# Kernel tuning notes

Measured on AMD Instinct MI355X. Metric: run time of the kernel, lower is better.

## Reference

```python
import jax, jax.numpy as jnp
import numpy as np

M, K, N = 131072, 1024, 512


def setup_inputs() -> dict:
    key = jax.random.key(0)
    k1, k2, k3, k4, k5 = jax.random.split(key, 5)
    scale = 0.02
    return {
        "x": jax.random.normal(k1, (M, K), dtype=jnp.float32),
        "w0": jax.random.uniform(k2, (K,), dtype=jnp.float32, minval=0.9, maxval=1.1),
        "w1": jax.random.normal(k3, (K, N), dtype=jnp.float32) * scale,
        "w2": jax.random.normal(k4, (K, N), dtype=jnp.float32) * scale,
        "w3": jax.random.normal(k5, (N, K), dtype=jnp.float32) * scale,
    }


def reference(x, w0, w1, w2, w3):
    # RMSNorm (no eps, matching the kernel): l = rsqrt(mean(x^2))
    l = jax.lax.rsqrt(jnp.sum(x * x, axis=-1) / K)          # [M]
    x1 = x * l[:, None] * w0[None, :]                        # [M, K]
    x2 = x1 @ w1                                             # gate   [M, N]
    y2 = x1 @ w2                                             # up     [M, N]
    x3 = jax.nn.silu(x2) * y2                                # SiLU-gate [M, N]
    out = x3 @ w3                                            # down   [M, K] (skip_connection=False)
    return out
```

## Files before the change

kernel.cpp:

```cpp
#include <hip/hip_runtime.h>
#include <cstdint>

typedef __attribute__((ext_vector_type(4))) float f32x4;
typedef __attribute__((ext_vector_type(8))) short bf16x8;
typedef __attribute__((ext_vector_type(4))) short bf16x4;

#define DEV static __device__ __forceinline__

DEV unsigned short f2bf(float f) {
    union { float f; unsigned int u; } v; v.f = f;
    unsigned int u = v.u;
    return (unsigned short)((u + 0x7FFFu + ((u >> 16) & 1u)) >> 16);
}

DEV void async_cp16(const void* g, void* l) {
    __builtin_amdgcn_global_load_lds(
        (const __attribute__((address_space(1))) unsigned int*)g,
        (__attribute__((address_space(3))) unsigned int*)l,
        16, 0, 0);
}

DEV void stage_half(const unsigned short* __restrict__ g, long kofs,
                    unsigned short* l, int tid, int gpitch) {
#pragma unroll
    for (int i = 0; i < 2; ++i) {
        int c = i * 512 + tid;
        int row = c >> 3;
        int ss = (c & 7) ^ (row & 7);
        async_cp16(g + (long)row * gpitch + kofs + ss * 8,
                   l + (i * 512 + (tid & 448)) * 8);
    }
}

DEV bf16x8 ldsrd(const unsigned short* base, int r, int q) {
    return *(const bf16x8*)&base[r * 64 + ((q ^ (r & 7)) << 3)];
}

template <int NT>
DEV void gemm256(const unsigned short* __restrict__ gA,
                 const unsigned short* __restrict__ gB,
                 const int gpitch, unsigned short* lds,
                 f32x4 (&acc)[8][4], const int tid) {
    const int lane = tid & 63;
    const int wv = tid >> 6;
    const int wr = wv >> 2;
    const int wcq = wv & 3;
    const int lhi = lane >> 4, llo = lane & 15;
    const int hb = wcq >> 1;
    const int br0 = (wcq & 1) * 64;

    const unsigned short* lA0 = lds + (0 * 2 + wr) * 8192;
    const unsigned short* lA1 = lds + (1 * 2 + wr) * 8192;
    const unsigned short* lB0 = lds + 32768 + (0 * 2 + hb) * 8192;
    const unsigned short* lB1 = lds + 32768 + (1 * 2 + hb) * 8192;

#define MG(AF, BF, RI0, CJ0)                                                  \
    _Pragma("unroll") for (int kq = 0; kq < 2; ++kq)                          \
    _Pragma("unroll") for (int i = 0; i < 4; ++i)                             \
    _Pragma("unroll") for (int j = 0; j < 2; ++j)                             \
        acc[RI0 + i][CJ0 + j] = __builtin_amdgcn_mfma_f32_16x16x32_bf16(      \
            AF[kq][i], BF[kq][j], acc[RI0 + i][CJ0 + j], 0, 0, 0);

#define RD_AF0(L) _Pragma("unroll") for (int kq = 0; kq < 2; ++kq)            \
    _Pragma("unroll") for (int i = 0; i < 4; ++i)                             \
        af0[kq][i] = ldsrd(L, i * 16 + llo, kq * 4 + lhi);
#define RD_AF1(L) _Pragma("unroll") for (int kq = 0; kq < 2; ++kq)            \
    _Pragma("unroll") for (int i = 0; i < 4; ++i)                             \
        af1[kq][i] = ldsrd(L, 64 + i * 16 + llo, kq * 4 + lhi);
#define RD_BF0(L) _Pragma("unroll") for (int kq = 0; kq < 2; ++kq)            \
    _Pragma("unroll") for (int j = 0; j < 2; ++j)                             \
        bf0[kq][j] = ldsrd(L, br0 + j * 16 + llo, kq * 4 + lhi);
#define RD_BF1(L) _Pragma("unroll") for (int kq = 0; kq < 2; ++kq)            \
    _Pragma("unroll") for (int j = 0; j < 2; ++j)                             \
        bf1[kq][j] = ldsrd(L, br0 + 32 + j * 16 + llo, kq * 4 + lhi);

#define SA0(BUF, K) stage_half(gA, K, lds + ((BUF) * 2 + 0) * 8192, tid, gpitch);
#define SA1(BUF, K) stage_half(gA + (long)128 * gpitch, K, lds + ((BUF) * 2 + 1) * 8192, tid, gpitch);
#define SB0(BUF, K) stage_half(gB, K, lds + 32768 + ((BUF) * 2 + 0) * 8192, tid, gpitch);
#define SB1(BUF, K) stage_half(gB + (long)128 * gpitch, K, lds + 32768 + ((BUF) * 2 + 1) * 8192, tid, gpitch);

#define BAR __builtin_amdgcn_s_barrier();
#define SCB __builtin_amdgcn_sched_barrier(0);
#define LGKM0 asm volatile("s_waitcnt lgkmcnt(0)");
#define P1 __builtin_amdgcn_s_setprio(1);
#define P0 __builtin_amdgcn_s_setprio(0);
#define VM2 asm volatile("s_waitcnt vmcnt(2)" ::: "memory");
#define VM0 asm volatile("s_waitcnt vmcnt(0)" ::: "memory");

    SA0(0, 0) SA1(0, 0) SB0(0, 0) SB1(0, 0)
    SA0(1, 64)
    VM2
    BAR

    bf16x8 af0[2][4], af1[2][4], bf0[2][2], bf1[2][2];

    for (int it = 0; it < NT / 2; ++it) {
        const long kO  = (long)(2 * it + 1) * 64;
        const long kE2 = (long)(2 * it + 2) * 64;
        const long kO2 = (long)(2 * it + 3) * 64;
        const bool pf = (it + 1 < NT / 2);

        RD_AF0(lA0) RD_BF0(lB0)
        SA1(1, kO)
        BAR LGKM0 SCB
        P1 MG(af0, bf0, 0, 0) P0
        BAR
        RD_BF1(lB0)
        SB0(1, kO)
        BAR LGKM0 SCB
        P1 MG(af0, bf1, 0, 2) P0
        BAR
        RD_AF1(lA0)
        SB1(1, kO)
        BAR LGKM0 SCB
        P1 MG(af1, bf0, 4, 0) P0
        BAR
        if (pf) { SA0(0, kE2) }
        BAR
        P1 MG(af1, bf1, 4, 2) P0
        if (pf) { VM2 } else { VM0 }
        BAR SCB

        RD_AF0(lA1) RD_BF0(lB1)
        if (pf) { SA1(0, kE2) }
        BAR LGKM0 SCB
        P1 MG(af0, bf0, 0, 0) P0
        BAR
        RD_BF1(lB1)
        if (pf) { SB0(0, kE2) }
        BAR LGKM0 SCB
        P1 MG(af0, bf1, 0, 2) P0
        BAR
        RD_AF1(lA1)
        if (pf) { SB1(0, kE2) }
        BAR LGKM0 SCB
        P1 MG(af1, bf0, 4, 0) P0
        BAR
        if (pf) { SA0(1, kO2) }
        BAR
        P1 MG(af1, bf1, 4, 2) P0
        if (pf) { VM2 }
        BAR SCB
    }
#undef MG
#undef RD_AF0
#undef RD_AF1
#undef RD_BF0
#undef RD_BF1
#undef SA0
#undef SA1
#undef SB0
#undef SB1
#undef BAR
#undef SCB
#undef LGKM0
#undef P1
#undef P0
#undef VM2
#undef VM0
}

__global__ void prep_w(const float* __restrict__ w0, const float* __restrict__ w1,
                       const float* __restrict__ w2, const float* __restrict__ w3,
                       unsigned short* __restrict__ w12t, unsigned short* __restrict__ w3t) {
    int t = blockIdx.x * 256 + threadIdx.x;
    if (t < 1048576) {
        int n = t >> 10, k = t & 1023;
        const float* src = (n & 1) ? w2 : w1;
        w12t[t] = f2bf(w0[k] * src[k * 512 + (n >> 1)]);
    } else {
        int idx = t - 1048576;
        int j = idx >> 9, n = idx & 511;
        w3t[idx] = f2bf(w3[n * 1024 + j]);
    }
}

__global__ __launch_bounds__(256)
void prep_x(const float* __restrict__ x, unsigned short* __restrict__ xb) {
    const int wv = threadIdx.x >> 6, lane = threadIdx.x & 63;
    const int stride = gridDim.x * 4;
    for (int row = blockIdx.x * 4 + wv; row < 131072; row += stride) {
        const float* xr = x + (long)row * 1024;
        f32x4 v[4];
        float s = 0.f;
#pragma unroll
        for (int c = 0; c < 4; ++c) {
            v[c] = *(const f32x4*)(xr + c * 256 + lane * 4);
            s += v[c].x * v[c].x + v[c].y * v[c].y + v[c].z * v[c].z + v[c].w * v[c].w;
        }
#pragma unroll
        for (int off = 32; off > 0; off >>= 1) s += __shfl_xor(s, off, 64);
        float l = rsqrtf(s * (1.0f / 1024.0f));
        unsigned short* xo = xb + (long)row * 1024;
#pragma unroll
        for (int c = 0; c < 4; ++c) {
            bf16x4 b;
            b.x = (short)f2bf(v[c].x * l);
            b.y = (short)f2bf(v[c].y * l);
            b.z = (short)f2bf(v[c].z * l);
            b.w = (short)f2bf(v[c].w * l);
            *(bf16x4*)(xo + c * 256 + lane * 4) = b;
        }
    }
}

__global__ __launch_bounds__(512, 2)
void gate_gemm(const unsigned short* __restrict__ xb,
               const unsigned short* __restrict__ w12t,
               unsigned short* __restrict__ x3) {
    __shared__ unsigned short lds[65536];
    const int tid = threadIdx.x;
    const int lane = tid & 63;
    const int wv = tid >> 6;
    const int wr = wv >> 2, wcq = wv & 3;
    const int lhi = lane >> 4, llo = lane & 15;

    int bid = blockIdx.x;
    int wgid = (bid & 7) * 256 + (bid >> 3);
    const int mt = wgid >> 2, nt = wgid & 3;

    f32x4 acc[8][4];
#pragma unroll
    for (int i = 0; i < 8; ++i)
#pragma unroll
        for (int j = 0; j < 4; ++j) acc[i][j] = (f32x4){0.f, 0.f, 0.f, 0.f};

    gemm256<16>(xb + (long)mt * 256 * 1024, w12t + (long)nt * 256 * 1024,
                1024, lds, acc, tid);

#pragma unroll
    for (int ri = 0; ri < 8; ++ri)
#pragma unroll
        for (int rr = 0; rr < 4; ++rr) {
            int R = wr * 128 + ri * 16 + lhi * 4 + rr;
#pragma unroll
            for (int cj = 0; cj < 4; ++cj) {
                float v = acc[ri][cj][rr];
                float p = __shfl_xor(v, 1, 64);
                float g = (lane & 1) ? p : v;
                float u = (lane & 1) ? v : p;
                float s = (g / (1.0f + __expf(-g))) * u;
                if (!(lane & 1))
                    lds[R * 136 + wcq * 32 + cj * 8 + (llo >> 1)] = f2bf(s);
            }
        }
    __syncthreads();
    unsigned short* xg = x3 + (long)(mt * 256) * 512 + nt * 128;
#pragma unroll
    for (int i = 0; i < 8; ++i) {
        int c = i * 512 + tid;
        int row = c >> 4, ch = c & 15;
        *(bf16x8*)(xg + (long)row * 512 + ch * 8) = *(const bf16x8*)&lds[row * 136 + ch * 8];
    }
}

__global__ __launch_bounds__(512, 2)
void down_gemm(const unsigned short* __restrict__ x3,
               const unsigned short* __restrict__ w3t,
               float* __restrict__ out) {
    __shared__ unsigned short lds[65536];
    const int tid = threadIdx.x;
    const int lane = tid & 63;
    const int wv = tid >> 6;
    const int wr = wv >> 2, wcq = wv & 3;
    const int lhi = lane >> 4, llo = lane & 15;

    int bid = blockIdx.x;
    int wgid = (bid & 7) * 256 + (bid >> 3);
    const int mt = wgid >> 2, nt = wgid & 3;

    f32x4 acc[8][4];
#pragma unroll
    for (int i = 0; i < 8; ++i)
#pragma unroll
        for (int j = 0; j < 4; ++j) acc[i][j] = (f32x4){0.f, 0.f, 0.f, 0.f};

    gemm256<8>(x3 + (long)mt * 256 * 512, w3t + (long)nt * 256 * 512,
               512, lds, acc, tid);

    float* op = out + (long)(mt * 256) * 1024 + nt * 256;
#pragma unroll
    for (int ri = 0; ri < 8; ++ri)
#pragma unroll
        for (int rr = 0; rr < 4; ++rr) {
            int R = wr * 128 + ri * 16 + lhi * 4 + rr;
#pragma unroll
            for (int cj = 0; cj < 4; ++cj)
                op[(long)R * 1024 + wcq * 64 + cj * 16 + llo] = acc[ri][cj][rr];
        }
}

extern "C" void kernel_launch(void* const* d_in, const int* in_sizes, int n_in,
                              void* d_out, int out_size, void* d_ws, size_t ws_size,
                              hipStream_t stream) {
    const float* x  = (const float*)d_in[0];
    const float* w0 = (const float*)d_in[1];
    const float* w1 = (const float*)d_in[2];
    const float* w2 = (const float*)d_in[3];
    const float* w3 = (const float*)d_in[4];
    float* out = (float*)d_out;

    unsigned short* w12t = (unsigned short*)d_ws;
    unsigned short* w3t  = w12t + 1024 * 1024;
    unsigned short* x3   = w3t + 1024 * 512;
    unsigned short* xb   = x3 + (size_t)131072 * 512;

    prep_w<<<dim3(6144), dim3(256), 0, stream>>>(w0, w1, w2, w3, w12t, w3t);
    prep_x<<<dim3(2048), dim3(256), 0, stream>>>(x, xb);
    gate_gemm<<<dim3(2048), dim3(512), 0, stream>>>(xb, w12t, x3);
    down_gemm<<<dim3(2048), dim3(512), 0, stream>>>(x3, w3t, out);
}
```

Measured before the change: 697.7 us.

## Fuse RMSNorm prep into gate GEMM by loading fp32 x and converting in-kernel

Removes the separate prep_x kernel. The gate GEMM now loads fp32 x rows directly into registers, converts them to bf16, and writes them into swizzled LDS while accumulating the sum of squares. The per-row rsqrt scale is applied to the accumulators after the GEMM, before the SiLU gate. This eliminates the bf16 xb round trip through HBM (one write plus one read), but each of the four N-tile blocks now reads fp32 x, doubling A-side read bytes, and the pipeline waits on vmcnt(0) each tile, which reduces overlap.

```diff
diff --git a/kernel.cpp b/kernel.cpp
--- a/kernel.cpp
+++ b/kernel.cpp
@@ -1,9 +1,11 @@
 #include <hip/hip_runtime.h>
+#include <hip/hip_bf16.h>
 #include <cstdint>
 
 typedef __attribute__((ext_vector_type(4))) float f32x4;
 typedef __attribute__((ext_vector_type(8))) short bf16x8;
 typedef __attribute__((ext_vector_type(4))) short bf16x4;
+typedef __attribute__((ext_vector_type(4))) unsigned int u32x4;
 
 #define DEV static __device__ __forceinline__
 
@@ -11,6 +13,10 @@
     union { float f; unsigned int u; } v; v.f = f;
     unsigned int u = v.u;
     return (unsigned short)((u + 0x7FFFu + ((u >> 16) & 1u)) >> 16);
+}
+
+DEV unsigned int pkbf(float a, float b) {
+    return ((unsigned int)f2bf(b) << 16) | f2bf(a);
 }
 
 DEV void async_cp16(const void* g, void* l) {
@@ -35,6 +41,35 @@
 DEV bf16x8 ldsrd(const unsigned short* base, int r, int q) {
     return *(const bf16x8*)&base[r * 64 + ((q ^ (r & 7)) << 3)];
 }
+
+#define BAR __builtin_amdgcn_s_barrier();
+#define SCB __builtin_amdgcn_sched_barrier(0);
+#define LGKM0 asm volatile("s_waitcnt lgkmcnt(0)");
+#define P1 __builtin_amdgcn_s_setprio(1);
+#define P0 __builtin_amdgcn_s_setprio(0);
+#define VM0 asm volatile("s_waitcnt vmcnt(0)" ::: "memory");
+#define VM2 asm volatile("s_waitcnt vmcnt(2)" ::: "memory");
+#define VM8 asm volatile("s_waitcnt vmcnt(8)" ::: "memory");
+
+#define MG(AF, BF, RI0, CJ0)                                                  \
+    _Pragma("unroll") for (int kq = 0; kq < 2; ++kq)                          \
+    _Pragma("unroll") for (int i = 0; i < 4; ++i)                             \
+    _Pragma("unroll") for (int j = 0; j < 2; ++j)                             \
+        acc[RI0 + i][CJ0 + j] = __builtin_amdgcn_mfma_f32_16x16x32_bf16(      \
+            AF[kq][i], BF[kq][j], acc[RI0 + i][CJ0 + j], 0, 0, 0);
+
+#define RD_AF0(L) _Pragma("unroll") for (int kq = 0; kq < 2; ++kq)            \
+    _Pragma("unroll") for (int i = 0; i < 4; ++i)                             \
+        af0[kq][i] = ldsrd(L, i * 16 + llo, kq * 4 + lhi);
+#define RD_AF1(L) _Pragma("unroll") for (int kq = 0; kq < 2; ++kq)            \
+    _Pragma("unroll") for (int i = 0; i < 4; ++i)                             \
+        af1[kq][i] = ldsrd(L, 64 + i * 16 + llo, kq * 4 + lhi);
+#define RD_BF0(L) _Pragma("unroll") for (int kq = 0; kq < 2; ++kq)            \
+    _Pragma("unroll") for (int j = 0; j < 2; ++j)                             \
+        bf0[kq][j] = ldsrd(L, br0 + j * 16 + llo, kq * 4 + lhi);
+#define RD_BF1(L) _Pragma("unroll") for (int kq = 0; kq < 2; ++kq)            \
+    _Pragma("unroll") for (int j = 0; j < 2; ++j)                             \
+        bf1[kq][j] = ldsrd(L, br0 + 32 + j * 16 + llo, kq * 4 + lhi);
 
 template <int NT>
 DEV void gemm256(const unsigned short* __restrict__ gA,
@@ -54,38 +89,10 @@
     const unsigned short* lB0 = lds + 32768 + (0 * 2 + hb) * 8192;
     const unsigned short* lB1 = lds + 32768 + (1 * 2 + hb) * 8192;
 
-#define MG(AF, BF, RI0, CJ0)                                                  \
-    _Pragma("unroll") for (int kq = 0; kq < 2; ++kq)                          \
-    _Pragma("unroll") for (int i = 0; i < 4; ++i)                             \
-    _Pragma("unroll") for (int j = 0; j < 2; ++j)                             \
-        acc[RI0 + i][CJ0 + j] = __builtin_amdgcn_mfma_f32_16x16x32_bf16(      \
-            AF[kq][i], BF[kq][j], acc[RI0 + i][CJ0 + j], 0, 0, 0);
-
-#define RD_AF0(L) _Pragma("unroll") for (int kq = 0; kq < 2; ++kq)            \
-    _Pragma("unroll") for (int i = 0; i < 4; ++i)                             \
-        af0[kq][i] = ldsrd(L, i * 16 + llo, kq * 4 + lhi);
-#define RD_AF1(L) _Pragma("unroll") for (int kq = 0; kq < 2; ++kq)            \
-    _Pragma("unroll") for (int i = 0; i < 4; ++i)                             \
-        af1[kq][i] = ldsrd(L, 64 + i * 16 + llo, kq * 4 + lhi);
-#define RD_BF0(L) _Pragma("unroll") for (int kq = 0; kq < 2; ++kq)            \
-    _Pragma("unroll") for (int j = 0; j < 2; ++j)                             \
-        bf0[kq][j] = ldsrd(L, br0 + j * 16 + llo, kq * 4 + lhi);
-#define RD_BF1(L) _Pragma("unroll") for (int kq = 0; kq < 2; ++kq)            \
-    _Pragma("unroll") for (int j = 0; j < 2; ++j)                             \
-        bf1[kq][j] = ldsrd(L, br0 + 32 + j * 16 + llo, kq * 4 + lhi);
-
 #define SA0(BUF, K) stage_half(gA, K, lds + ((BUF) * 2 + 0) * 8192, tid, gpitch);
 #define SA1(BUF, K) stage_half(gA + (long)128 * gpitch, K, lds + ((BUF) * 2 + 1) * 8192, tid, gpitch);
 #define SB0(BUF, K) stage_half(gB, K, lds + 32768 + ((BUF) * 2 + 0) * 8192, tid, gpitch);
 #define SB1(BUF, K) stage_half(gB + (long)128 * gpitch, K, lds + 32768 + ((BUF) * 2 + 1) * 8192, tid, gpitch);
-
-#define BAR __builtin_amdgcn_s_barrier();
-#define SCB __builtin_amdgcn_sched_barrier(0);
-#define LGKM0 asm volatile("s_waitcnt lgkmcnt(0)");
-#define P1 __builtin_amdgcn_s_setprio(1);
-#define P0 __builtin_amdgcn_s_setprio(0);
-#define VM2 asm volatile("s_waitcnt vmcnt(2)" ::: "memory");
-#define VM0 asm volatile("s_waitcnt vmcnt(0)" ::: "memory");
 
     SA0(0, 0) SA1(0, 0) SB0(0, 0) SB1(0, 0)
     SA0(1, 64)
@@ -142,22 +149,10 @@
         if (pf) { VM2 }
         BAR SCB
     }
-#undef MG
-#undef RD_AF0
-#undef RD_AF1
-#undef RD_BF0
-#undef RD_BF1
 #undef SA0
 #undef SA1
 #undef SB0
 #undef SB1
-#undef BAR
-#undef SCB
-#undef LGKM0
-#undef P1
-#undef P0
-#undef VM2
-#undef VM0
 }
 
 __global__ void prep_w(const float* __restrict__ w0, const float* __restrict__ w1,
@@ -175,67 +170,133 @@
     }
 }
 
-__global__ __launch_bounds__(256)
-void prep_x(const float* __restrict__ x, unsigned short* __restrict__ xb) {
-    const int wv = threadIdx.x >> 6, lane = threadIdx.x & 63;
-    const int stride = gridDim.x * 4;
-    for (int row = blockIdx.x * 4 + wv; row < 131072; row += stride) {
-        const float* xr = x + (long)row * 1024;
-        f32x4 v[4];
-        float s = 0.f;
-#pragma unroll
-        for (int c = 0; c < 4; ++c) {
-            v[c] = *(const f32x4*)(xr + c * 256 + lane * 4);
-            s += v[c].x * v[c].x + v[c].y * v[c].y + v[c].z * v[c].z + v[c].w * v[c].w;
-        }
-#pragma unroll
-        for (int off = 32; off > 0; off >>= 1) s += __shfl_xor(s, off, 64);
-        float l = rsqrtf(s * (1.0f / 1024.0f));
-        unsigned short* xo = xb + (long)row * 1024;
-#pragma unroll
-        for (int c = 0; c < 4; ++c) {
-            bf16x4 b;
-            b.x = (short)f2bf(v[c].x * l);
-            b.y = (short)f2bf(v[c].y * l);
-            b.z = (short)f2bf(v[c].z * l);
-            b.w = (short)f2bf(v[c].w * l);
-            *(bf16x4*)(xo + c * 256 + lane * 4) = b;
-        }
-    }
-}
-
 __global__ __launch_bounds__(512, 2)
-void gate_gemm(const unsigned short* __restrict__ xb,
+void gate_gemm(const float* __restrict__ x,
                const unsigned short* __restrict__ w12t,
                unsigned short* __restrict__ x3) {
     __shared__ unsigned short lds[65536];
+    __shared__ float spart[1024];
+    __shared__ float lrow[256];
+
     const int tid = threadIdx.x;
     const int lane = tid & 63;
     const int wv = tid >> 6;
     const int wr = wv >> 2, wcq = wv & 3;
     const int lhi = lane >> 4, llo = lane & 15;
+    const int hb = wcq >> 1;
+    const int br0 = (wcq & 1) * 64;
 
     int bid = blockIdx.x;
     int wgid = (bid & 7) * 256 + (bid >> 3);
     const int mt = wgid >> 2, nt = wgid & 3;
 
+    const unsigned short* gB = w12t + (long)nt * 256 * 1024;
+    const int arow = tid >> 2;
+    const int acol = tid & 3;
+    const float* gxr0 = x + (long)(mt * 256 + arow) * 1024 + acol * 16;
+    const float* gxr1 = gxr0 + (long)128 * 1024;
+    const int ws0 = (((acol * 2)     ^ (arow & 7)) << 3);
+    const int ws1 = (((acol * 2 + 1) ^ (arow & 7)) << 3);
+
+    f32x4 ar[2][4];
+    float sq0 = 0.f, sq1 = 0.f;
+
+#define ALOAD(KOFS) { _Pragma("unroll") for (int c = 0; c < 4; ++c) {          \
+        ar[0][c] = *(const f32x4*)(gxr0 + (KOFS) + c * 4);                     \
+        ar[1][c] = *(const f32x4*)(gxr1 + (KOFS) + c * 4); } }
+
+#define ACVT(D) { _Pragma("unroll") for (int h2 = 0; h2 < 2; ++h2) {           \
+        float s = 0.f; unsigned int pk[8];                                     \
+        _Pragma("unroll") for (int c = 0; c < 4; ++c) {                        \
+            f32x4 v = ar[h2][c];                                               \
+            s += v.x * v.x + v.y * v.y + v.z * v.z + v.w * v.w;                \
+            pk[c * 2]     = pkbf(v.x, v.y);                                    \
+            pk[c * 2 + 1] = pkbf(v.z, v.w); }                                  \
+        if (h2 == 0) sq0 += s; else sq1 += s;                                  \
+        unsigned short* dst = lds + ((D) * 2 + h2) * 8192 + arow * 64;         \
+        *(u32x4*)(dst + ws0) = (u32x4){pk[0], pk[1], pk[2], pk[3]};            \
+        *(u32x4*)(dst + ws1) = (u32x4){pk[4], pk[5], pk[6], pk[7]}; } }
+
+#define SB0G(BUF, K) stage_half(gB, K, lds + 32768 + ((BUF) * 2 + 0) * 8192, tid, 1024);
+#define SB1G(BUF, K) stage_half(gB + (long)128 * 1024, K, lds + 32768 + ((BUF) * 2 + 1) * 8192, tid, 1024);
+
     f32x4 acc[8][4];
 #pragma unroll
     for (int i = 0; i < 8; ++i)
 #pragma unroll
         for (int j = 0; j < 4; ++j) acc[i][j] = (f32x4){0.f, 0.f, 0.f, 0.f};
 
-    gemm256<16>(xb + (long)mt * 256 * 1024, w12t + (long)nt * 256 * 1024,
-                1024, lds, acc, tid);
+    ALOAD(0)
+    SB0G(0, 0) SB1G(0, 0)
+    ACVT(0)
+    ALOAD(64)
+    LGKM0
+    VM8
+    BAR SCB
+
+    bf16x8 af0[2][4], af1[2][4], bf0[2][2], bf1[2][2];
+
+#define GTILE(CUR, NXT, T)                                                     \
+    {                                                                          \
+        const unsigned short* lA = lds + ((CUR) * 2 + wr) * 8192;              \
+        const unsigned short* lB = lds + 32768 + ((CUR) * 2 + hb) * 8192;      \
+        const bool pf = (T) + 1 < 16;                                          \
+        const bool al = ((T) >= 1) && pf;                                      \
+        const long k1 = (long)((T) + 1) * 64;                                  \
+                                                                      \
+        RD_AF0(lA) RD_BF0(lB)                                                  \
+        BAR LGKM0 SCB                                                          \
+        P1 MG(af0, bf0, 0, 0) P0                                               \
+        BAR                                                                    \
+                                                                      \
+        RD_BF1(lB)                                                             \
+        if (pf) { SB0G(NXT, k1) SB1G(NXT, k1) }                                \
+        BAR LGKM0 SCB                                                          \
+        P1 MG(af0, bf1, 0, 2) P0                                               \
+        BAR                                                                    \
+                                                                      \
+        RD_AF1(lA)                                                             \
+        if (al) { ALOAD(k1 * 1) }                                              \
+        BAR LGKM0 SCB                                                          \
+        P1 MG(af1, bf0, 4, 0) P0                                               \
+        BAR                                                                    \
+                                                                      \
+        P1 MG(af1, bf1, 4, 2) P0                                               \
+        if (pf) { ACVT(NXT) }                                                  \
+        LGKM0                                                                  \
+        if (pf) { VM0 }                                                        \
+        BAR SCB                                                                \
+    }
+
+#pragma unroll
+    for (int it = 0; it < 8; ++it) {
+        GTILE(0, 1, 2 * it)
+        GTILE(1, 0, 2 * it + 1)
+    }
+#undef GTILE
+#undef ALOAD
+#undef ACVT
+#undef SB0G
+#undef SB1G
+
+    spart[arow * 4 + acol] = sq0;
+    spart[(128 + arow) * 4 + acol] = sq1;
+    __syncthreads();
+    if (tid < 256) {
+        float s = spart[tid * 4] + spart[tid * 4 + 1] + spart[tid * 4 + 2] + spart[tid * 4 + 3];
+        lrow[tid] = rsqrtf(s * (1.0f / 1024.0f));
+    }
+    __syncthreads();
 
 #pragma unroll
     for (int ri = 0; ri < 8; ++ri)
 #pragma unroll
         for (int rr = 0; rr < 4; ++rr) {
             int R = wr * 128 + ri * 16 + lhi * 4 + rr;
+            float l = lrow[R];
 #pragma unroll
             for (int cj = 0; cj < 4; ++cj) {
-                float v = acc[ri][cj][rr];
+                float v = acc[ri][cj][rr] * l;
                 float p = __shfl_xor(v, 1, 64);
                 float g = (lane & 1) ? p : v;
                 float u = (lane & 1) ? v : p;
@@ -303,10 +364,8 @@
     unsigned short* w12t = (unsigned short*)d_ws;
     unsigned short* w3t  = w12t + 1024 * 1024;
     unsigned short* x3   = w3t + 1024 * 512;
-    unsigned short* xb   = x3 + (size_t)131072 * 512;
 
     prep_w<<<dim3(6144), dim3(256), 0, stream>>>(w0, w1, w2, w3, w12t, w3t);
-    prep_x<<<dim3(2048), dim3(256), 0, stream>>>(x, xb);
-    gate_gemm<<<dim3(2048), dim3(512), 0, stream>>>(xb, w12t, x3);
+    gate_gemm<<<dim3(2048), dim3(512), 0, stream>>>(x, w12t, x3);
     down_gemm<<<dim3(2048), dim3(512), 0, stream>>>(x3, w3t, out);
 }
```

Measured after the change: 906.1 us. 1.3x slower.

## Switch GEMM core to 32x32x16 bf16 MFMA with new LDS swizzle

Applied to the files above, without the earlier changes.

Replaces the 16x16x32 MFMA tiling with 32x32x16 bf16 MFMA instructions in the shared 256x256 GEMM core. Each wave now holds 4x2 32x32 accumulators. The LDS swizzle gains an extra XOR term so the new 32-lane read pattern avoids bank conflicts. Both epilogues are remapped to the new accumulator layout. The intent is fewer MFMA issues and LDS reads per FLOP, at the cost of changed register pressure and more complex index mapping.

```diff
diff --git a/kernel.cpp b/kernel.cpp
--- a/kernel.cpp
+++ b/kernel.cpp
@@ -2,6 +2,7 @@
 #include <cstdint>
 
 typedef __attribute__((ext_vector_type(4))) float f32x4;
+typedef __attribute__((ext_vector_type(16))) float f32x16;
 typedef __attribute__((ext_vector_type(8))) short bf16x8;
 typedef __attribute__((ext_vector_type(4))) short bf16x4;
 
@@ -20,79 +21,81 @@
         16, 0, 0);
 }
 
-DEV void stage_half(const unsigned short* __restrict__ g, long kofs,
-                    unsigned short* l, int tid, int gpitch) {
-#pragma unroll
-    for (int i = 0; i < 2; ++i) {
-        int c = i * 512 + tid;
-        int row = c >> 3;
-        int ss = (c & 7) ^ (row & 7);
-        async_cp16(g + (long)row * gpitch + kofs + ss * 8,
-                   l + (i * 512 + (tid & 448)) * 8);
-    }
-}
-
-DEV bf16x8 ldsrd(const unsigned short* base, int r, int q) {
-    return *(const bf16x8*)&base[r * 64 + ((q ^ (r & 7)) << 3)];
-}
-
-template <int NT>
-DEV void gemm256(const unsigned short* __restrict__ gA,
-                 const unsigned short* __restrict__ gB,
-                 const int gpitch, unsigned short* lds,
-                 f32x4 (&acc)[8][4], const int tid) {
-    const int lane = tid & 63;
-    const int wv = tid >> 6;
-    const int wr = wv >> 2;
-    const int wcq = wv & 3;
-    const int lhi = lane >> 4, llo = lane & 15;
-    const int hb = wcq >> 1;
-    const int br0 = (wcq & 1) * 64;
-
-    const unsigned short* lA0 = lds + (0 * 2 + wr) * 8192;
-    const unsigned short* lA1 = lds + (1 * 2 + wr) * 8192;
-    const unsigned short* lB0 = lds + 32768 + (0 * 2 + hb) * 8192;
-    const unsigned short* lB1 = lds + 32768 + (1 * 2 + hb) * 8192;
-
-#define MG(AF, BF, RI0, CJ0)                                                  \
-    _Pragma("unroll") for (int kq = 0; kq < 2; ++kq)                          \
-    _Pragma("unroll") for (int i = 0; i < 4; ++i)                             \
-    _Pragma("unroll") for (int j = 0; j < 2; ++j)                             \
-        acc[RI0 + i][CJ0 + j] = __builtin_amdgcn_mfma_f32_16x16x32_bf16(      \
-            AF[kq][i], BF[kq][j], acc[RI0 + i][CJ0 + j], 0, 0, 0);
-
-#define RD_AF0(L) _Pragma("unroll") for (int kq = 0; kq < 2; ++kq)            \
-    _Pragma("unroll") for (int i = 0; i < 4; ++i)                             \
-        af0[kq][i] = ldsrd(L, i * 16 + llo, kq * 4 + lhi);
-#define RD_AF1(L) _Pragma("unroll") for (int kq = 0; kq < 2; ++kq)            \
-    _Pragma("unroll") for (int i = 0; i < 4; ++i)                             \
-        af1[kq][i] = ldsrd(L, 64 + i * 16 + llo, kq * 4 + lhi);
-#define RD_BF0(L) _Pragma("unroll") for (int kq = 0; kq < 2; ++kq)            \
-    _Pragma("unroll") for (int j = 0; j < 2; ++j)                             \
-        bf0[kq][j] = ldsrd(L, br0 + j * 16 + llo, kq * 4 + lhi);
-#define RD_BF1(L) _Pragma("unroll") for (int kq = 0; kq < 2; ++kq)            \
-    _Pragma("unroll") for (int j = 0; j < 2; ++j)                             \
-        bf1[kq][j] = ldsrd(L, br0 + 32 + j * 16 + llo, kq * 4 + lhi);
-
-#define SA0(BUF, K) stage_half(gA, K, lds + ((BUF) * 2 + 0) * 8192, tid, gpitch);
-#define SA1(BUF, K) stage_half(gA + (long)128 * gpitch, K, lds + ((BUF) * 2 + 1) * 8192, tid, gpitch);
-#define SB0(BUF, K) stage_half(gB, K, lds + 32768 + ((BUF) * 2 + 0) * 8192, tid, gpitch);
-#define SB1(BUF, K) stage_half(gB + (long)128 * gpitch, K, lds + 32768 + ((BUF) * 2 + 1) * 8192, tid, gpitch);
-
 #define BAR __builtin_amdgcn_s_barrier();
 #define SCB __builtin_amdgcn_sched_barrier(0);
 #define LGKM0 asm volatile("s_waitcnt lgkmcnt(0)");
 #define P1 __builtin_amdgcn_s_setprio(1);
 #define P0 __builtin_amdgcn_s_setprio(0);
+#define VM0 asm volatile("s_waitcnt vmcnt(0)" ::: "memory");
 #define VM2 asm volatile("s_waitcnt vmcnt(2)" ::: "memory");
-#define VM0 asm volatile("s_waitcnt vmcnt(0)" ::: "memory");
+
+DEV void stage_half(const unsigned short* __restrict__ g, long kofs,
+                    unsigned short* l, int tid, int gpitch) {
+#pragma unroll
+    for (int i = 0; i < 2; ++i) {
+        int c = i * 512 + tid;
+        int row = c >> 3;
+        int ss = (c & 7) ^ (row & 7) ^ ((row >> 3) & 3);
+        async_cp16(g + (long)row * gpitch + kofs + ss * 8,
+                   l + (i * 512 + (tid & 448)) * 8);
+    }
+}
+
+template <int NT>
+DEV void gemm256(const unsigned short* __restrict__ gA,
+                 const unsigned short* __restrict__ gB,
+                 const int gpitch, unsigned short* lds,
+                 f32x16 (&acc)[4][2], const int tid) {
+    const int lane = tid & 63;
+    const int wv = tid >> 6;
+    const int wr = wv >> 2, wcq = wv & 3;
+    const int lw = lane & 31, hi5 = lane >> 5;
+    const int hb = wcq >> 1;
+    const int brq = wcq & 1;
+    const int F = (lw & 7) ^ ((lw >> 3) & 3);
+
+    const char* lb = (const char*)lds;
+    int oA[4], oB[4];
+#pragma unroll
+    for (int ks = 0; ks < 4; ++ks) {
+        int q = (((ks * 2 + hi5) ^ F) << 4);
+        oA[ks] = wr * 16384 + lw * 128 + q;
+        oB[ks] = 65536 + hb * 16384 + brq * 8192 + lw * 128 + q;
+    }
+
+#define LD8(OFF) (*(const bf16x8*)(lb + (OFF)))
+#define RD_AF(MB, CO) _Pragma("unroll") for (int ks = 0; ks < 4; ++ks) {      \
+        af[0][ks] = LD8(oA[ks] + (CO) + (MB) * 4096);                         \
+        af[1][ks] = LD8(oA[ks] + (CO) + (MB) * 4096 + 4096); }
+#define RD_BFA(CO) _Pragma("unroll") for (int ks = 0; ks < 2; ++ks) {         \
+        bfA[0][ks] = LD8(oB[ks] + (CO));                                      \
+        bfA[1][ks] = LD8(oB[ks] + (CO) + 4096); }
+#define RD_BFB(CO) _Pragma("unroll") for (int ks = 0; ks < 2; ++ks) {         \
+        bfB[0][ks] = LD8(oB[ks + 2] + (CO));                                  \
+        bfB[1][ks] = LD8(oB[ks + 2] + (CO) + 4096); }
+
+#define MM(B_, KB0, MOFF)                                                     \
+    _Pragma("unroll") for (int ks = 0; ks < 2; ++ks)                          \
+    _Pragma("unroll") for (int m = 0; m < 2; ++m)                             \
+    _Pragma("unroll") for (int n = 0; n < 2; ++n)                             \
+        acc[(MOFF) + m][n] = __builtin_amdgcn_mfma_f32_32x32x16_bf16(         \
+            af[m][(KB0) + ks], B_[n][ks], acc[(MOFF) + m][n], 0, 0, 0);
+
+#define SA0(BUF, K) stage_half(gA, K, lds + ((BUF) * 2 + 0) * 8192, tid, gpitch);
+#define SA1(BUF, K) stage_half(gA + (long)128 * gpitch, K, lds + ((BUF) * 2 + 1) * 8192, tid, gpitch);
+#define SB0(BUF, K) stage_half(gB, K, lds + 32768 + ((BUF) * 2 + 0) * 8192, tid, gpitch);
+#define SB1(BUF, K) stage_half(gB + (long)128 * gpitch, K, lds + 32768 + ((BUF) * 2 + 1) * 8192, tid, gpitch);
 
     SA0(0, 0) SA1(0, 0) SB0(0, 0) SB1(0, 0)
-    SA0(1, 64)
-    VM2
-    BAR
-
-    bf16x8 af0[2][4], af1[2][4], bf0[2][2], bf1[2][2];
+    if (NT > 1) {
+        SA0(1, 64)
+        VM2
+    } else {
+        VM0
+    }
+    BAR SCB
+
+    bf16x8 af[2][4], bfA[2][2], bfB[2][2];
 
     for (int it = 0; it < NT / 2; ++it) {
         const long kO  = (long)(2 * it + 1) * 64;
@@ -100,64 +103,57 @@
         const long kO2 = (long)(2 * it + 3) * 64;
         const bool pf = (it + 1 < NT / 2);
 
-        RD_AF0(lA0) RD_BF0(lB0)
+        RD_AF(0, 0) RD_BFA(0)
         SA1(1, kO)
         BAR LGKM0 SCB
-        P1 MG(af0, bf0, 0, 0) P0
-        BAR
-        RD_BF1(lB0)
+        P1 MM(bfA, 0, 0) P0
+        BAR
+        RD_BFB(0)
         SB0(1, kO)
         BAR LGKM0 SCB
-        P1 MG(af0, bf1, 0, 2) P0
-        BAR
-        RD_AF1(lA0)
+        P1 MM(bfB, 2, 0) P0
+        BAR
+        RD_AF(2, 0)
         SB1(1, kO)
         BAR LGKM0 SCB
-        P1 MG(af1, bf0, 4, 0) P0
+        P1 MM(bfA, 0, 2) P0
         BAR
         if (pf) { SA0(0, kE2) }
         BAR
-        P1 MG(af1, bf1, 4, 2) P0
+        P1 MM(bfB, 2, 2) P0
         if (pf) { VM2 } else { VM0 }
         BAR SCB
 
-        RD_AF0(lA1) RD_BF0(lB1)
+        RD_AF(0, 32768) RD_BFA(32768)
         if (pf) { SA1(0, kE2) }
         BAR LGKM0 SCB
-        P1 MG(af0, bf0, 0, 0) P0
-        BAR
-        RD_BF1(lB1)
+        P1 MM(bfA, 0, 0) P0
+        BAR
+        RD_BFB(32768)
         if (pf) { SB0(0, kE2) }
         BAR LGKM0 SCB
-        P1 MG(af0, bf1, 0, 2) P0
-        BAR
-        RD_AF1(lA1)
+        P1 MM(bfB, 2, 0) P0
+        BAR
+        RD_AF(2, 32768)
         if (pf) { SB1(0, kE2) }
         BAR LGKM0 SCB
-        P1 MG(af1, bf0, 4, 0) P0
+        P1 MM(bfA, 0, 2) P0
         BAR
         if (pf) { SA0(1, kO2) }
         BAR
-        P1 MG(af1, bf1, 4, 2) P0
+        P1 MM(bfB, 2, 2) P0
         if (pf) { VM2 }
         BAR SCB
     }
-#undef MG
-#undef RD_AF0
-#undef RD_AF1
-#undef RD_BF0
-#undef RD_BF1
+#undef MM
+#undef LD8
+#undef RD_AF
+#undef RD_BFA
+#undef RD_BFB
 #undef SA0
 #undef SA1
 #undef SB0
 #undef SB1
-#undef BAR
-#undef SCB
-#undef LGKM0
-#undef P1
-#undef P0
-#undef VM2
-#undef VM0
 }
 
 __global__ void prep_w(const float* __restrict__ w0, const float* __restrict__ w1,
@@ -213,37 +209,38 @@
     const int lane = tid & 63;
     const int wv = tid >> 6;
     const int wr = wv >> 2, wcq = wv & 3;
-    const int lhi = lane >> 4, llo = lane & 15;
+    const int lw = lane & 31, hi5 = lane >> 5;
 
     int bid = blockIdx.x;
     int wgid = (bid & 7) * 256 + (bid >> 3);
     const int mt = wgid >> 2, nt = wgid & 3;
 
-    f32x4 acc[8][4];
-#pragma unroll
-    for (int i = 0; i < 8; ++i)
-#pragma unroll
-        for (int j = 0; j < 4; ++j) acc[i][j] = (f32x4){0.f, 0.f, 0.f, 0.f};
+    f32x16 acc[4][2];
+#pragma unroll
+    for (int i = 0; i < 4; ++i)
+#pragma unroll
+        for (int j = 0; j < 2; ++j)
+#pragma unroll
+            for (int r = 0; r < 16; ++r) acc[i][j][r] = 0.f;
 
     gemm256<16>(xb + (long)mt * 256 * 1024, w12t + (long)nt * 256 * 1024,
                 1024, lds, acc, tid);
 
 #pragma unroll
-    for (int ri = 0; ri < 8; ++ri)
-#pragma unroll
-        for (int rr = 0; rr < 4; ++rr) {
-            int R = wr * 128 + ri * 16 + lhi * 4 + rr;
-#pragma unroll
-            for (int cj = 0; cj < 4; ++cj) {
-                float v = acc[ri][cj][rr];
+    for (int m = 0; m < 4; ++m)
+#pragma unroll
+        for (int n = 0; n < 2; ++n)
+#pragma unroll
+            for (int reg = 0; reg < 16; ++reg) {
+                int R = wr * 128 + m * 32 + (reg & 3) + (reg >> 2) * 8 + hi5 * 4;
+                float v = acc[m][n][reg];
                 float p = __shfl_xor(v, 1, 64);
                 float g = (lane & 1) ? p : v;
                 float u = (lane & 1) ? v : p;
                 float s = (g / (1.0f + __expf(-g))) * u;
                 if (!(lane & 1))
-                    lds[R * 136 + wcq * 32 + cj * 8 + (llo >> 1)] = f2bf(s);
+                    lds[R * 136 + wcq * 32 + n * 16 + (lw >> 1)] = f2bf(s);
             }
-        }
     __syncthreads();
     unsigned short* xg = x3 + (long)(mt * 256) * 512 + nt * 128;
 #pragma unroll
@@ -263,31 +260,33 @@
     const int lane = tid & 63;
     const int wv = tid >> 6;
     const int wr = wv >> 2, wcq = wv & 3;
-    const int lhi = lane >> 4, llo = lane & 15;
+    const int lw = lane & 31, hi5 = lane >> 5;
 
     int bid = blockIdx.x;
     int wgid = (bid & 7) * 256 + (bid >> 3);
     const int mt = wgid >> 2, nt = wgid & 3;
 
-    f32x4 acc[8][4];
-#pragma unroll
-    for (int i = 0; i < 8; ++i)
-#pragma unroll
-        for (int j = 0; j < 4; ++j) acc[i][j] = (f32x4){0.f, 0.f, 0.f, 0.f};
+    f32x16 acc[4][2];
+#pragma unroll
+    for (int i = 0; i < 4; ++i)
+#pragma unroll
+        for (int j = 0; j < 2; ++j)
+#pragma unroll
+            for (int r = 0; r < 16; ++r) acc[i][j][r] = 0.f;
 
     gemm256<8>(x3 + (long)mt * 256 * 512, w3t + (long)nt * 256 * 512,
                512, lds, acc, tid);
 
     float* op = out + (long)(mt * 256) * 1024 + nt * 256;
 #pragma unroll
-    for (int ri = 0; ri < 8; ++ri)
-#pragma unroll
-        for (int rr = 0; rr < 4; ++rr) {
-            int R = wr * 128 + ri * 16 + lhi * 4 + rr;
-#pragma unroll
-            for (int cj = 0; cj < 4; ++cj)
-                op[(long)R * 1024 + wcq * 64 + cj * 16 + llo] = acc[ri][cj][rr];
-        }
+    for (int m = 0; m < 4; ++m)
+#pragma unroll
+        for (int n = 0; n < 2; ++n)
+#pragma unroll
+            for (int reg = 0; reg < 16; ++reg) {
+                int R = wr * 128 + m * 32 + (reg & 3) + (reg >> 2) * 8 + hi5 * 4;
+                op[(long)R * 1024 + wcq * 64 + n * 32 + lw] = acc[m][n][reg];
+            }
 }
 
 extern "C" void kernel_launch(void* const* d_in, const int* in_sizes, int n_in,
```

Measured after the change: 743.8 us. 6.6% more time.
